# Kernel optimization log

Measured on AMD Instinct MI355X. Metric: run time of the kernel, lower is better.

Reference implementation:

```python
import jax, jax.numpy as jnp
import numpy as np

IN_DIM = 512
REDUCED = IN_DIM // 8  # reduction_ratio = 8
B, C, H, W = 8, 32, 64, IN_DIM


def setup_inputs() -> dict:
    key = jax.random.key(0)
    ks = jax.random.split(key, 9)
    s_in = 1.0 / np.sqrt(IN_DIM)
    inp = {
        "x": jax.random.normal(ks[0], (B, C, H, W), dtype=jnp.float32),
        # torch Linear weights stored here as [in, out] for y = x @ w + b
        "wq": jax.random.uniform(ks[1], (IN_DIM, REDUCED), jnp.float32, -s_in, s_in),
        "bq": jax.random.uniform(ks[2], (REDUCED,), jnp.float32, -s_in, s_in),
        "wk": jax.random.uniform(ks[3], (IN_DIM, REDUCED), jnp.float32, -s_in, s_in),
        "bk": jax.random.uniform(ks[4], (REDUCED,), jnp.float32, -s_in, s_in),
        "wv": jax.random.uniform(ks[5], (IN_DIM, IN_DIM), jnp.float32, -s_in, s_in),
        "bv": jax.random.uniform(ks[6], (IN_DIM,), jnp.float32, -s_in, s_in),
        "wo": jax.random.uniform(ks[7], (IN_DIM, IN_DIM), jnp.float32, -s_in, s_in),
        "bo": jax.random.uniform(ks[8], (IN_DIM,), jnp.float32, -s_in, s_in),
    }
    return inp


def reference(x, wq, bq, wk, bk, wv, bv, wo, bo):
    b, c, h, w = x.shape
    n = c * h  # attention tokens = flattened C*H positions, feature dim = W
    q = (x @ wq + bq).reshape(b, n, REDUCED)   # [B, N, r]
    k = (x @ wk + bk).reshape(b, n, REDUCED)   # [B, N, r]
    v = (x @ wv + bv).reshape(b, n, w)         # [B, N, W]
    energy = jnp.einsum("bnr,bmr->bnm", q, k)  # [B, N, N]
    attn = jax.nn.softmax(energy, axis=-1)
    out = jnp.einsum("bnm,bmd->bnd", attn, v).reshape(b, c, h, w)
    out = out @ wo + bo
    return out + x
```

## Files before the change

kernel.cpp:

```cpp
#include <hip/hip_runtime.h>

typedef __bf16 bf16x8 __attribute__((ext_vector_type(8)));
typedef float  f32x4  __attribute__((ext_vector_type(4)));

union U8 { uint4 v; unsigned short u[8]; };

static __device__ __forceinline__ float bf2f(unsigned short u) {
    union { unsigned int i; float f; } c; c.i = ((unsigned int)u) << 16; return c.f;
}
static __device__ __forceinline__ unsigned short f2bf(float f) {
    union { float f; unsigned int i; } c; c.f = f;
    unsigned int x = c.i;
    unsigned int r = (x + 0x7FFFu + ((x >> 16) & 1u)) >> 16;
    return (unsigned short)r;
}

static __device__ __forceinline__ U8 load8(const float* p) {
    U8 r;
    const float4 a = *(const float4*)p;
    const float4 b = *(const float4*)(p + 4);
    r.u[0] = f2bf(a.x); r.u[1] = f2bf(a.y); r.u[2] = f2bf(a.z); r.u[3] = f2bf(a.w);
    r.u[4] = f2bf(b.x); r.u[5] = f2bf(b.y); r.u[6] = f2bf(b.z); r.u[7] = f2bf(b.w);
    return r;
}

static __device__ __forceinline__ void gld_lds16(const void* g, void* l) {
    __builtin_amdgcn_global_load_lds(
        (const __attribute__((address_space(1))) unsigned int*)g,
        (__attribute__((address_space(3))) unsigned int*)l, 16, 0, 0);
}

__global__ __launch_bounds__(256)
void pack(const float* __restrict__ x, unsigned short* __restrict__ xb,
          const float* __restrict__ bq, const float* __restrict__ bk,
          const float* __restrict__ bv, float* __restrict__ ball,
          const float* __restrict__ wv, const float* __restrict__ wo,
          const float* __restrict__ wq, const float* __restrict__ wk,
          unsigned short* __restrict__ wAllT, unsigned short* __restrict__ woT)
{
    const int bid = blockIdx.x, t = threadIdx.x;
    if (bid < 2048) {
        const long i = ((long)bid * 256 + t) * 16;
        U8 a = load8(x + i);
        U8 b = load8(x + i + 8);
        *(uint4*)(xb + i) = a.v;
        *(uint4*)(xb + i + 8) = b.v;
        if (bid == 0) {
            ball[t]       = t < 64 ? bq[t] : (t < 128 ? bk[t - 64] : bv[t - 128]);
            ball[t + 256] = bv[t + 128];
            if (t < 128) ball[t + 512] = bv[t + 384];
        }
        return;
    }
    __shared__ float sT[64][65];
    const int b2 = bid - 2048;
    const int zz = b2 >> 6, rem = b2 & 63;
    const int cx = rem & 7, ry = rem >> 3;
    const float* src; unsigned short* dst; int C;
    if      (zz == 0) { src = wv; dst = wAllT + 128 * 512; C = 512; }
    else if (zz == 1) { src = wo; dst = woT;               C = 512; }
    else if (zz == 2) { src = wq; dst = wAllT;             C = 64;  }
    else              { src = wk; dst = wAllT + 64 * 512;  C = 64;  }
    const int R = 512;
    const int c0 = cx * 64, r0 = ry * 64;
    if (c0 >= C) return;
    #pragma unroll
    for (int k = 0; k < 16; ++k) {
        const int lin = k * 256 + t;
        const int i = lin >> 6, j = lin & 63;
        sT[i][j] = src[(long)(r0 + i) * C + c0 + j];
    }
    __syncthreads();
    #pragma unroll
    for (int k = 0; k < 16; ++k) {
        const int lin = k * 256 + t;
        const int o = lin >> 6, i2 = lin & 63;
        dst[(long)(c0 + o) * R + r0 + i2] = f2bf(sT[i2][o]);
    }
}

template<bool BIAS, bool RES, bool OUT_F32, bool MIXED, int NCOL>
__global__ __launch_bounds__(256, 3)
void gemm64(const unsigned short* __restrict__ A, int lda,
            const unsigned short* __restrict__ B, int ldb,
            void* __restrict__ Cp, int ldc,
            void* __restrict__ Cp2,
            const float* __restrict__ bias,
            const float* __restrict__ resid,
            int K)
{
    __shared__ __align__(16) unsigned short sMem[2][12288];

    const int t = threadIdx.x, wave = t >> 6, lane = t & 63;
    const int lr = lane & 15, quad = lane >> 4;

    const int bid = blockIdx.x;
    const int sw  = (bid & 7) * (NCOL * 32) + (bid >> 3);
    const int rowBase = (sw / NCOL) * 64;
    const int colBase = (sw % NCOL) * 128;
    const int wm = (wave & 1) * 32, wn = (wave >> 1) * 64;

    const int srow  = lane >> 3;
    const int sslot = lane & 7;
    const int swz   = (sslot ^ srow) << 4;

    f32x4 acc[2][4];
    #pragma unroll
    for (int mt = 0; mt < 2; ++mt)
        #pragma unroll
        for (int nt = 0; nt < 4; ++nt) acc[mt][nt] = (f32x4){0.f, 0.f, 0.f, 0.f};

    auto STAGE = [&](int buf, int kt) {
        unsigned short* sA = sMem[buf];
        unsigned short* sB = sMem[buf] + 4096;
        #pragma unroll
        for (int is = 0; is < 2; ++is) {
            const int r0 = wave * 16 + is * 8;
            gld_lds16((const char*)A + ((long)(rowBase + r0 + srow) * lda + kt) * 2 + swz,
                      (char*)sA + r0 * 128);
        }
        #pragma unroll
        for (int is = 0; is < 4; ++is) {
            const int r0 = wave * 32 + is * 8;
            gld_lds16((const char*)B + ((long)(colBase + r0 + srow) * ldb + kt) * 2 + swz,
                      (char*)sB + r0 * 128);
        }
    };

    STAGE(0, 0);
    __syncthreads();

    int cur = 0;
    for (int kt = 0; kt < K; kt += 64) {
        if (kt + 64 < K) STAGE(cur ^ 1, kt + 64);

        const unsigned short* sA = sMem[cur];
        const unsigned short* sB = sMem[cur] + 4096;
        #pragma unroll
        for (int ks = 0; ks < 2; ++ks) {
            const int kb = ks * 64 + quad * 16;
            bf16x8 bfr[4];
            #pragma unroll
            for (int nt = 0; nt < 4; ++nt) {
                const int row = wn + nt * 16 + lr;
                bfr[nt] = *(const bf16x8*)((const char*)sB + row * 128 + (kb ^ ((row & 7) << 4)));
            }
            #pragma unroll
            for (int mt = 0; mt < 2; ++mt) {
                const int row = wm + mt * 16 + lr;
                bf16x8 af = *(const bf16x8*)((const char*)sA + row * 128 + (kb ^ ((row & 7) << 4)));
                #pragma unroll
                for (int nt = 0; nt < 4; ++nt)
                    acc[mt][nt] = __builtin_amdgcn_mfma_f32_16x16x32_bf16(af, bfr[nt], acc[mt][nt], 0, 0, 0);
            }
        }
        __syncthreads();
        cur ^= 1;
    }

    if (MIXED && colBase >= 128) {
        unsigned short* sT = sMem[0];
        #pragma unroll
        for (int mt = 0; mt < 2; ++mt)
            #pragma unroll
            for (int nt = 0; nt < 4; ++nt) {
                const int row0 = wm + mt * 16 + quad * 4;
                const int col  = wn + nt * 16 + lr;
                const float b = BIAS ? bias[colBase + col] : 0.f;
                ushort4 v4;
                v4.x = f2bf(acc[mt][nt][0] + b);
                v4.y = f2bf(acc[mt][nt][1] + b);
                v4.z = f2bf(acc[mt][nt][2] + b);
                v4.w = f2bf(acc[mt][nt][3] + b);
                *(ushort4*)&sT[col * 72 + row0] = v4;
            }
        __syncthreads();
        unsigned short* C2 = (unsigned short*)Cp2;
        const int bat = rowBase >> 11, key0 = rowBase & 2047;
        const long vcol0 = colBase - 128;
        #pragma unroll
        for (int ro = 0; ro < 4; ++ro) {
            const int flat = ro * 256 + t;
            const int col = flat >> 3, ch = flat & 7;
            const uint4 v = *(const uint4*)&sT[col * 72 + ch * 8];
            *(uint4*)&C2[((long)bat * 512 + vcol0 + col) * 2048 + key0 + ch * 8] = v;
        }
        return;
    }

    float* Cf = (float*)Cp;
    unsigned short* Cb = (unsigned short*)Cp;
    #pragma unroll
    for (int mt = 0; mt < 2; ++mt)
        #pragma unroll
        for (int nt = 0; nt < 4; ++nt) {
            const int row0 = rowBase + wm + mt * 16 + quad * 4;
            const int col  = colBase + wn + nt * 16 + lr;
            const float b = BIAS ? bias[col] : 0.f;
            #pragma unroll
            for (int r = 0; r < 4; ++r) {
                const int row = row0 + r;
                float v = acc[mt][nt][r] + b;
                if (RES)     v += resid[(long)row * ldc + col];
                if (OUT_F32) Cf[(long)row * ldc + col] = v;
                else         Cb[(long)row * ldc + col] = f2bf(v);
            }
        }
}

__global__ __launch_bounds__(512, 4)
void flash_attn(const unsigned short* __restrict__ QK,
                const unsigned short* __restrict__ VT,
                unsigned short* __restrict__ O)
{
    __shared__ __align__(16) unsigned short sK[2][64 * 64];
    __shared__ __align__(16) unsigned short sP[2][64 * 72];
    __shared__ float sL[64];

    const int bid = blockIdx.x;
    const int z  = bid & 7;
    const int rr = bid >> 3;
    const int cs = rr & 1;
    const int qt = rr >> 1;

    const int t = threadIdx.x, wave = t >> 6, lane = t & 63;
    const int lr = lane & 15, quad = lane >> 4;
    const int sw = wave & 3;
    const bool isS = wave < 4;

    const long qrow0 = (long)z * 2048 + qt * 64;
    bf16x8 qa0, qa1;
    if (isS) {
        const unsigned short* qp = QK + (qrow0 + sw * 16 + lr) * 128 + quad * 8;
        qa0 = *(const bf16x8*)(qp);
        qa1 = *(const bf16x8*)(qp + 32);
    }

    const char* Kb = (const char*)(QK + (long)z * 2048 * 128 + 64);
    const unsigned short* Vb = VT + (long)z * 512 * 2048
                                  + ((long)cs * 256 + wave * 32) * 2048;

    const long stg_go = (long)(sw * 16 + (lane >> 3)) * 256
                      + (((lane & 7) ^ (lane >> 3)) << 4);
    const int swq = (lr & 7) << 4;

    f32x4 acc[4][2];
    #pragma unroll
    for (int mt = 0; mt < 4; ++mt)
        #pragma unroll
        for (int nt = 0; nt < 2; ++nt) acc[mt][nt] = (f32x4){0.f, 0.f, 0.f, 0.f};
    float lsum[4] = {0.f, 0.f, 0.f, 0.f};

    if (!isS) {
        const char* gk = Kb + stg_go;
        char* lk = (char*)sK[0] + sw * 2048;
        gld_lds16(gk, lk);
        gld_lds16(gk + 2048, lk + 1024);
    }
    __syncthreads();

    int cur = 0;
    for (int kt = 0; kt < 32; ++kt) {
        const int key0 = kt * 64;

        bf16x8 vv[2][2];
        #pragma unroll
        for (int nt = 0; nt < 2; ++nt) {
            const unsigned short* vp = Vb + (long)(nt * 16 + lr) * 2048 + key0 + quad * 8;
            vv[nt][0] = *(const bf16x8*)(vp);
            vv[nt][1] = *(const bf16x8*)(vp + 32);
        }

        if (!isS) {
            if (kt < 31) {
                const char* gk = Kb + (long)(kt + 1) * 16384 + stg_go;
                char* lk = (char*)sK[cur ^ 1] + sw * 2048;
                gld_lds16(gk, lk);
                gld_lds16(gk + 2048, lk + 1024);
            }
        } else {
            const char* sKc = (const char*)sK[cur];
            __bf16* sPb = (__bf16*)sP[cur];
            #pragma unroll
            for (int nt = 0; nt < 4; ++nt) {
                const int kb = (nt * 16 + lr) * 128;
                bf16x8 k0 = *(const bf16x8*)(sKc + kb + ((quad * 16) ^ swq));
                bf16x8 k1 = *(const bf16x8*)(sKc + kb + ((quad * 16 + 64) ^ swq));
                f32x4 sv = (f32x4){0.f, 0.f, 0.f, 0.f};
                sv = __builtin_amdgcn_mfma_f32_16x16x32_bf16(qa0, k0, sv, 0, 0, 0);
                sv = __builtin_amdgcn_mfma_f32_16x16x32_bf16(qa1, k1, sv, 0, 0, 0);
                #pragma unroll
                for (int r = 0; r < 4; ++r) {
                    const float e = __expf(sv[r]);
                    const __bf16 pb = (__bf16)e;
                    lsum[r] += (float)pb;
                    sPb[(sw * 16 + quad * 4 + r) * 72 + nt * 16 + lr] = pb;
                }
            }
        }

        __syncthreads();

        const unsigned short* sPc = sP[cur];
        __builtin_amdgcn_s_setprio(1);
        #pragma unroll
        for (int mt = 0; mt < 4; ++mt) {
            const unsigned short* pp = &sPc[(mt * 16 + lr) * 72 + quad * 8];
            bf16x8 p0 = *(const bf16x8*)(pp);
            bf16x8 p1 = *(const bf16x8*)(pp + 32);
            acc[mt][0] = __builtin_amdgcn_mfma_f32_16x16x32_bf16(p0, vv[0][0], acc[mt][0], 0, 0, 0);
            acc[mt][0] = __builtin_amdgcn_mfma_f32_16x16x32_bf16(p1, vv[0][1], acc[mt][0], 0, 0, 0);
            acc[mt][1] = __builtin_amdgcn_mfma_f32_16x16x32_bf16(p0, vv[1][0], acc[mt][1], 0, 0, 0);
            acc[mt][1] = __builtin_amdgcn_mfma_f32_16x16x32_bf16(p1, vv[1][1], acc[mt][1], 0, 0, 0);
        }
        __builtin_amdgcn_s_setprio(0);
        cur ^= 1;
    }

    if (isS) {
        #pragma unroll
        for (int r = 0; r < 4; ++r) {
            float v = lsum[r];
            v += __shfl_xor(v, 1); v += __shfl_xor(v, 2);
            v += __shfl_xor(v, 4); v += __shfl_xor(v, 8);
            lsum[r] = v;
        }
        if (lr == 0) {
            #pragma unroll
            for (int r = 0; r < 4; ++r) sL[sw * 16 + quad * 4 + r] = lsum[r];
        }
    }
    __syncthreads();

    #pragma unroll
    for (int mt = 0; mt < 4; ++mt) {
        float inv[4];
        #pragma unroll
        for (int r = 0; r < 4; ++r) inv[r] = 1.0f / sL[mt * 16 + quad * 4 + r];
        #pragma unroll
        for (int nt = 0; nt < 2; ++nt) {
            const int col = cs * 256 + wave * 32 + nt * 16 + lr;
            #pragma unroll
            for (int r = 0; r < 4; ++r) {
                const long row = qrow0 + mt * 16 + quad * 4 + r;
                O[row * 512 + col] = f2bf(acc[mt][nt][r] * inv[r]);
            }
        }
    }
}

extern "C" void kernel_launch(void* const* d_in, const int* in_sizes, int n_in,
                              void* d_out, int out_size, void* d_ws, size_t ws_size,
                              hipStream_t stream)
{
    const float* x  = (const float*)d_in[0];
    const float* wq = (const float*)d_in[1];
    const float* bq = (const float*)d_in[2];
    const float* wk = (const float*)d_in[3];
    const float* bk = (const float*)d_in[4];
    const float* wv = (const float*)d_in[5];
    const float* bv = (const float*)d_in[6];
    const float* wo = (const float*)d_in[7];
    const float* bo = (const float*)d_in[8];

    const int W = 512;
    float* out = (float*)d_out;
    dim3 blk(256);
    char* ws = (char*)d_ws;

    const size_t NEED = 56ull << 20;
    if (ws_size < NEED) return;

    unsigned short* QK    = (unsigned short*)(ws);
    unsigned short* VT    = (unsigned short*)(ws + ( 4ull << 20));
    unsigned short* O     = (unsigned short*)(ws + (20ull << 20));
    unsigned short* xb    = (unsigned short*)(ws + (36ull << 20));
    unsigned short* wAllT = (unsigned short*)(ws + (52ull << 20));
    unsigned short* woT   = (unsigned short*)(ws + (53ull << 20));
    float*          ball  = (float*)         (ws + (53ull << 20) + (512ull << 10));

    pack<<<dim3(2048 + 256), blk, 0, stream>>>(x, xb, bq, bk, bv, ball,
                                               wv, wo, wq, wk, wAllT, woT);

    gemm64<true, false, false, true, 5><<<dim3(1280), blk, 0, stream>>>(
        xb, W, wAllT, W, QK, 128, VT, ball, nullptr, W);

    flash_attn<<<dim3(512), dim3(512), 0, stream>>>(QK, VT, O);

    gemm64<true, true, true, false, 4><<<dim3(1024), blk, 0, stream>>>(
        O, W, woT, W, out, W, nullptr, bo, x, W);
}
```

Before: 203.8 us.

## Load K directly from global memory and XOR-swizzle the P tile in LDS

```diff
diff --git a/kernel.cpp b/kernel.cpp
--- a/kernel.cpp
+++ b/kernel.cpp
@@ -213,7 +213,6 @@
                 const unsigned short* __restrict__ VT,
                 unsigned short* __restrict__ O)
 {
-    __shared__ __align__(16) unsigned short sK[2][64 * 64];
     __shared__ __align__(16) unsigned short sP[2][64 * 72];
     __shared__ float sL[64];
 
@@ -240,9 +239,8 @@
     const unsigned short* Vb = VT + (long)z * 512 * 2048
                                   + ((long)cs * 256 + wave * 32) * 2048;
 
-    const long stg_go = (long)(sw * 16 + (lane >> 3)) * 256
-                      + (((lane & 7) ^ (lane >> 3)) << 4);
-    const int swq = (lr & 7) << 4;
+    const int wsw = quad << 4;
+    const int rsw = (lr >> 2) << 4;
 
     f32x4 acc[4][2];
     #pragma unroll
@@ -250,14 +248,6 @@
         #pragma unroll
         for (int nt = 0; nt < 2; ++nt) acc[mt][nt] = (f32x4){0.f, 0.f, 0.f, 0.f};
     float lsum[4] = {0.f, 0.f, 0.f, 0.f};
-
-    if (!isS) {
-        const char* gk = Kb + stg_go;
-        char* lk = (char*)sK[0] + sw * 2048;
-        gld_lds16(gk, lk);
-        gld_lds16(gk + 2048, lk + 1024);
-    }
-    __syncthreads();
 
     int cur = 0;
     for (int kt = 0; kt < 32; ++kt) {
@@ -271,21 +261,13 @@
             vv[nt][1] = *(const bf16x8*)(vp + 32);
         }
 
-        if (!isS) {
-            if (kt < 31) {
-                const char* gk = Kb + (long)(kt + 1) * 16384 + stg_go;
-                char* lk = (char*)sK[cur ^ 1] + sw * 2048;
-                gld_lds16(gk, lk);
-                gld_lds16(gk + 2048, lk + 1024);
-            }
-        } else {
-            const char* sKc = (const char*)sK[cur];
+        if (isS) {
             __bf16* sPb = (__bf16*)sP[cur];
             #pragma unroll
             for (int nt = 0; nt < 4; ++nt) {
-                const int kb = (nt * 16 + lr) * 128;
-                bf16x8 k0 = *(const bf16x8*)(sKc + kb + ((quad * 16) ^ swq));
-                bf16x8 k1 = *(const bf16x8*)(sKc + kb + ((quad * 16 + 64) ^ swq));
+                const char* kp = Kb + (long)(key0 + nt * 16 + lr) * 256 + quad * 16;
+                bf16x8 k0 = *(const bf16x8*)(kp);
+                bf16x8 k1 = *(const bf16x8*)(kp + 64);
                 f32x4 sv = (f32x4){0.f, 0.f, 0.f, 0.f};
                 sv = __builtin_amdgcn_mfma_f32_16x16x32_bf16(qa0, k0, sv, 0, 0, 0);
                 sv = __builtin_amdgcn_mfma_f32_16x16x32_bf16(qa1, k1, sv, 0, 0, 0);
@@ -294,7 +276,7 @@
                     const float e = __expf(sv[r]);
                     const __bf16 pb = (__bf16)e;
                     lsum[r] += (float)pb;
-                    sPb[(sw * 16 + quad * 4 + r) * 72 + nt * 16 + lr] = pb;
+                    sPb[(sw * 16 + quad * 4 + r) * 72 + ((nt * 16 + lr) ^ wsw)] = pb;
                 }
             }
         }
@@ -305,9 +287,9 @@
         __builtin_amdgcn_s_setprio(1);
         #pragma unroll
         for (int mt = 0; mt < 4; ++mt) {
-            const unsigned short* pp = &sPc[(mt * 16 + lr) * 72 + quad * 8];
-            bf16x8 p0 = *(const bf16x8*)(pp);
-            bf16x8 p1 = *(const bf16x8*)(pp + 32);
+            const int rbase = (mt * 16 + lr) * 72;
+            bf16x8 p0 = *(const bf16x8*)&sPc[rbase + ((quad * 8) ^ rsw)];
+            bf16x8 p1 = *(const bf16x8*)&sPc[rbase + ((quad * 8 + 32) ^ rsw)];
             acc[mt][0] = __builtin_amdgcn_mfma_f32_16x16x32_bf16(p0, vv[0][0], acc[mt][0], 0, 0, 0);
             acc[mt][0] = __builtin_amdgcn_mfma_f32_16x16x32_bf16(p1, vv[0][1], acc[mt][0], 0, 0, 0);
             acc[mt][1] = __builtin_amdgcn_mfma_f32_16x16x32_bf16(p0, vv[1][0], acc[mt][1], 0, 0, 0);
```

Measured after the change: 257.6 us. 1.26x slower.

## Warp-specialize attention: score waves compute softmax one tile ahead, PV waves own output

Applied to the files above, without the earlier changes.

```diff
diff --git a/kernel.cpp b/kernel.cpp
--- a/kernel.cpp
+++ b/kernel.cpp
@@ -238,83 +238,87 @@
 
     const char* Kb = (const char*)(QK + (long)z * 2048 * 128 + 64);
     const unsigned short* Vb = VT + (long)z * 512 * 2048
-                                  + ((long)cs * 256 + wave * 32) * 2048;
+                                  + ((long)cs * 256 + sw * 64) * 2048;
 
     const long stg_go = (long)(sw * 16 + (lane >> 3)) * 256
                       + (((lane & 7) ^ (lane >> 3)) << 4);
     const int swq = (lr & 7) << 4;
 
-    f32x4 acc[4][2];
+    f32x4 acc[4][4];
     #pragma unroll
     for (int mt = 0; mt < 4; ++mt)
         #pragma unroll
-        for (int nt = 0; nt < 2; ++nt) acc[mt][nt] = (f32x4){0.f, 0.f, 0.f, 0.f};
+        for (int nt = 0; nt < 4; ++nt) acc[mt][nt] = (f32x4){0.f, 0.f, 0.f, 0.f};
     float lsum[4] = {0.f, 0.f, 0.f, 0.f};
 
-    if (!isS) {
+    auto SPHASE = [&](int tile) {
+        const char* sKc = (const char*)sK[tile & 1];
+        __bf16* sPb = (__bf16*)sP[tile & 1];
+        #pragma unroll
+        for (int nt = 0; nt < 4; ++nt) {
+            const int kb = (nt * 16 + lr) * 128;
+            bf16x8 k0 = *(const bf16x8*)(sKc + kb + ((quad * 16) ^ swq));
+            bf16x8 k1 = *(const bf16x8*)(sKc + kb + ((quad * 16 + 64) ^ swq));
+            f32x4 sv = (f32x4){0.f, 0.f, 0.f, 0.f};
+            sv = __builtin_amdgcn_mfma_f32_16x16x32_bf16(qa0, k0, sv, 0, 0, 0);
+            sv = __builtin_amdgcn_mfma_f32_16x16x32_bf16(qa1, k1, sv, 0, 0, 0);
+            #pragma unroll
+            for (int r = 0; r < 4; ++r) {
+                const float e = __expf(sv[r]);
+                const __bf16 pb = (__bf16)e;
+                lsum[r] += (float)pb;
+                sPb[(sw * 16 + quad * 4 + r) * 72 + nt * 16 + lr] = pb;
+            }
+        }
+    };
+
+    if (isS) {
         const char* gk = Kb + stg_go;
-        char* lk = (char*)sK[0] + sw * 2048;
-        gld_lds16(gk, lk);
-        gld_lds16(gk + 2048, lk + 1024);
-    }
-    __syncthreads();
-
-    int cur = 0;
+        char* lk0 = (char*)sK[0] + sw * 2048;
+        char* lk1 = (char*)sK[1] + sw * 2048;
+        gld_lds16(gk, lk0);
+        gld_lds16(gk + 2048, lk0 + 1024);
+        gld_lds16(gk + 16384, lk1);
+        gld_lds16(gk + 16384 + 2048, lk1 + 1024);
+    }
+    __syncthreads();
+    if (isS) SPHASE(0);
+    __syncthreads();
+
     for (int kt = 0; kt < 32; ++kt) {
-        const int key0 = kt * 64;
-
-        bf16x8 vv[2][2];
-        #pragma unroll
-        for (int nt = 0; nt < 2; ++nt) {
-            const unsigned short* vp = Vb + (long)(nt * 16 + lr) * 2048 + key0 + quad * 8;
-            vv[nt][0] = *(const bf16x8*)(vp);
-            vv[nt][1] = *(const bf16x8*)(vp + 32);
-        }
-
-        if (!isS) {
-            if (kt < 31) {
-                const char* gk = Kb + (long)(kt + 1) * 16384 + stg_go;
-                char* lk = (char*)sK[cur ^ 1] + sw * 2048;
+        if (isS) {
+            if (kt + 2 < 32) {
+                const char* gk = Kb + (long)(kt + 2) * 16384 + stg_go;
+                char* lk = (char*)sK[kt & 1] + sw * 2048;
                 gld_lds16(gk, lk);
                 gld_lds16(gk + 2048, lk + 1024);
             }
+            if (kt + 1 < 32) SPHASE(kt + 1);
         } else {
-            const char* sKc = (const char*)sK[cur];
-            __bf16* sPb = (__bf16*)sP[cur];
+            const int key0 = kt * 64;
+            bf16x8 vv[4][2];
             #pragma unroll
             for (int nt = 0; nt < 4; ++nt) {
-                const int kb = (nt * 16 + lr) * 128;
-                bf16x8 k0 = *(const bf16x8*)(sKc + kb + ((quad * 16) ^ swq));
-                bf16x8 k1 = *(const bf16x8*)(sKc + kb + ((quad * 16 + 64) ^ swq));
-                f32x4 sv = (f32x4){0.f, 0.f, 0.f, 0.f};
-                sv = __builtin_amdgcn_mfma_f32_16x16x32_bf16(qa0, k0, sv, 0, 0, 0);
-                sv = __builtin_amdgcn_mfma_f32_16x16x32_bf16(qa1, k1, sv, 0, 0, 0);
+                const unsigned short* vp = Vb + (long)(nt * 16 + lr) * 2048 + key0 + quad * 8;
+                vv[nt][0] = *(const bf16x8*)(vp);
+                vv[nt][1] = *(const bf16x8*)(vp + 32);
+            }
+            const unsigned short* sPc = sP[kt & 1];
+            __builtin_amdgcn_s_setprio(1);
+            #pragma unroll
+            for (int mt = 0; mt < 4; ++mt) {
+                const unsigned short* pp = &sPc[(mt * 16 + lr) * 72 + quad * 8];
+                bf16x8 p0 = *(const bf16x8*)(pp);
+                bf16x8 p1 = *(const bf16x8*)(pp + 32);
                 #pragma unroll
-                for (int r = 0; r < 4; ++r) {
-                    const float e = __expf(sv[r]);
-                    const __bf16 pb = (__bf16)e;
-                    lsum[r] += (float)pb;
-                    sPb[(sw * 16 + quad * 4 + r) * 72 + nt * 16 + lr] = pb;
+                for (int nt = 0; nt < 4; ++nt) {
+                    acc[mt][nt] = __builtin_amdgcn_mfma_f32_16x16x32_bf16(p0, vv[nt][0], acc[mt][nt], 0, 0, 0);
+                    acc[mt][nt] = __builtin_amdgcn_mfma_f32_16x16x32_bf16(p1, vv[nt][1], acc[mt][nt], 0, 0, 0);
                 }
             }
-        }
-
+            __builtin_amdgcn_s_setprio(0);
+        }
         __syncthreads();
-
-        const unsigned short* sPc = sP[cur];
-        __builtin_amdgcn_s_setprio(1);
-        #pragma unroll
-        for (int mt = 0; mt < 4; ++mt) {
-            const unsigned short* pp = &sPc[(mt * 16 + lr) * 72 + quad * 8];
-            bf16x8 p0 = *(const bf16x8*)(pp);
-            bf16x8 p1 = *(const bf16x8*)(pp + 32);
-            acc[mt][0] = __builtin_amdgcn_mfma_f32_16x16x32_bf16(p0, vv[0][0], acc[mt][0], 0, 0, 0);
-            acc[mt][0] = __builtin_amdgcn_mfma_f32_16x16x32_bf16(p1, vv[0][1], acc[mt][0], 0, 0, 0);
-            acc[mt][1] = __builtin_amdgcn_mfma_f32_16x16x32_bf16(p0, vv[1][0], acc[mt][1], 0, 0, 0);
-            acc[mt][1] = __builtin_amdgcn_mfma_f32_16x16x32_bf16(p1, vv[1][1], acc[mt][1], 0, 0, 0);
-        }
-        __builtin_amdgcn_s_setprio(0);
-        cur ^= 1;
     }
 
     if (isS) {
@@ -332,18 +336,20 @@
     }
     __syncthreads();
 
-    #pragma unroll
-    for (int mt = 0; mt < 4; ++mt) {
-        float inv[4];
-        #pragma unroll
-        for (int r = 0; r < 4; ++r) inv[r] = 1.0f / sL[mt * 16 + quad * 4 + r];
-        #pragma unroll
-        for (int nt = 0; nt < 2; ++nt) {
-            const int col = cs * 256 + wave * 32 + nt * 16 + lr;
-            #pragma unroll
-            for (int r = 0; r < 4; ++r) {
-                const long row = qrow0 + mt * 16 + quad * 4 + r;
-                O[row * 512 + col] = f2bf(acc[mt][nt][r] * inv[r]);
+    if (!isS) {
+        #pragma unroll
+        for (int mt = 0; mt < 4; ++mt) {
+            float inv[4];
+            #pragma unroll
+            for (int r = 0; r < 4; ++r) inv[r] = 1.0f / sL[mt * 16 + quad * 4 + r];
+            #pragma unroll
+            for (int nt = 0; nt < 4; ++nt) {
+                const int col = cs * 256 + sw * 64 + nt * 16 + lr;
+                #pragma unroll
+                for (int r = 0; r < 4; ++r) {
+                    const long row = qrow0 + mt * 16 + quad * 4 + r;
+                    O[row * 512 + col] = f2bf(acc[mt][nt][r] * inv[r]);
+                }
             }
         }
     }
```

Result: slower. 255.7 us (+25.5%).
